# Performance work log

Hardware: AMD Instinct MI355X
Metric: run time of the kernel (lower is better)

Reference implementation:

```python
import jax, jax.numpy as jnp
import numpy as np

N_HEAD = 32
N_KV_HEAD = 8
HEAD_DIM = 64
N_EMBD = 2048
B, T = 2, 2048
ROPE_BASE = 10000.0


def _rope_cos_sin(T, head_dim, dtype):
    pos = jnp.arange(T, dtype=jnp.float32)
    dim_arr = jnp.arange(0, head_dim, 2, dtype=jnp.float32)
    freqs = ROPE_BASE ** (-dim_arr / head_dim)
    theta = jnp.outer(pos, freqs)                      # [T, hd/2]
    cos = jnp.concatenate([jnp.cos(theta), jnp.cos(theta)], axis=-1)  # [T, hd]
    sin = jnp.concatenate([jnp.sin(theta), jnp.sin(theta)], axis=-1)
    # broadcast to [1, T, 1, hd]
    return cos[None, :, None, :].astype(dtype), sin[None, :, None, :].astype(dtype)


def _rotate_half(v):
    h = v.shape[-1] // 2
    return jnp.concatenate([-v[..., h:], v[..., :h]], axis=-1)


def setup_inputs() -> dict:
    key = jax.random.key(0)
    kx, kq, kk, kv, ko = jax.random.split(key, 5)
    s = 1.0 / np.sqrt(N_EMBD)
    return {
        "x": jax.random.normal(kx, (B, T, N_EMBD), dtype=jnp.float32),
        "wq": jax.random.normal(kq, (N_EMBD, N_HEAD * HEAD_DIM), dtype=jnp.float32) * s,
        "wk": jax.random.normal(kk, (N_EMBD, N_KV_HEAD * HEAD_DIM), dtype=jnp.float32) * s,
        "wv": jax.random.normal(kv, (N_EMBD, N_KV_HEAD * HEAD_DIM), dtype=jnp.float32) * s,
        "wo": jax.random.normal(ko, (N_HEAD * HEAD_DIM, N_EMBD), dtype=jnp.float32) * s,
    }


def reference(x, wq, wk, wv, wo):
    Bx, Tx, C = x.shape
    n_rep = N_HEAD // N_KV_HEAD

    xq = (x @ wq).reshape(Bx, Tx, N_HEAD, HEAD_DIM)
    xk = (x @ wk).reshape(Bx, Tx, N_KV_HEAD, HEAD_DIM)
    xv = (x @ wv).reshape(Bx, Tx, N_KV_HEAD, HEAD_DIM)

    cos, sin = _rope_cos_sin(Tx, HEAD_DIM, x.dtype)
    xq = xq * cos + _rotate_half(xq) * sin
    xk = xk * cos + _rotate_half(xk) * sin

    # GQA: repeat_interleave KV heads to match query heads
    xk = jnp.repeat(xk, n_rep, axis=2)  # [B, T, H, hd]
    xv = jnp.repeat(xv, n_rep, axis=2)

    scale = 1.0 / np.sqrt(HEAD_DIM)
    # scores: [B, H, T, T]
    scores = jnp.einsum("bqhd,bkhd->bhqk", xq, xk) * scale
    causal = jnp.tril(jnp.ones((Tx, Tx), dtype=bool))
    scores = jnp.where(causal[None, None], scores, -jnp.inf)
    probs = jax.nn.softmax(scores, axis=-1)

    out = jnp.einsum("bhqk,bkhd->bqhd", probs, xv).reshape(Bx, Tx, N_HEAD * HEAD_DIM)
    return out @ wo
```

## Files before the change

### kernel.cpp

```cpp
#include <hip/hip_runtime.h>
#include <hip/hip_bf16.h>
#include <cstdint>
#include <cstddef>

#define B_ 2
#define T_ 2048
#define H_ 32
#define KVH_ 8
#define D_ 64
#define C_ 2048
#define NQKV 3072

typedef short short8 __attribute__((ext_vector_type(8)));
typedef float f32x4 __attribute__((ext_vector_type(4)));
typedef unsigned short u16;

__device__ __forceinline__ u16 f2b(float f) {
  union { float f; unsigned u; } x; x.f = f;
  unsigned r = x.u + 0x7fffu + ((x.u >> 16) & 1u);
  return (u16)(r >> 16);
}

__device__ __forceinline__ float b2f(u16 v) {
  union { unsigned u; float f; } x; x.u = ((unsigned)v) << 16;
  return x.f;
}

__device__ __forceinline__ void gload16(const void* g, void* l) {
  __builtin_amdgcn_global_load_lds(
      (const __attribute__((address_space(1))) unsigned int*)g,
      (__attribute__((address_space(3))) unsigned int*)l,
      16, 0, 0);
}

__device__ __forceinline__ f32x4 mfma16(short8 a, short8 b, f32x4 c) {
  return __builtin_amdgcn_mfma_f32_16x16x32_bf16(a, b, c, 0, 0, 0);
}

__device__ __forceinline__ unsigned cvtpk(float lo_, float hi_) {
  unsigned r;
  asm("v_cvt_pk_bf16_f32 %0, %1, %2" : "=v"(r) : "v"(lo_), "v"(hi_));
  return r;
}

__global__ void k_tbl(float* __restrict__ tbl) {
  int i = blockIdx.x * 256 + threadIdx.x;
  int t = i >> 5, f = i & 31;
  double freq = pow(10000.0, -(double)f / 32.0);
  double th = (double)t * freq;
  tbl[i * 2 + 0] = (float)cos(th);
  tbl[i * 2 + 1] = (float)sin(th);
}

__global__ void k_cvtx(const float* __restrict__ x, u16* __restrict__ xb) {
  int i = blockIdx.x * 256 + threadIdx.x;
  float4 v = ((const float4*)x)[i];
  ushort4 o;
  o.x = f2b(v.x); o.y = f2b(v.y); o.z = f2b(v.z); o.w = f2b(v.w);
  ((ushort4*)xb)[i] = o;
}

__global__ void k_transw(const float* __restrict__ src, u16* __restrict__ dst, int N) {
  __shared__ float t[32][33];
  int tx = threadIdx.x, ty = threadIdx.y;
  int k0 = blockIdx.y * 32, n0 = blockIdx.x * 32;
#pragma unroll
  for (int i = 0; i < 4; i++)
    t[ty + i * 8][tx] = src[(size_t)(k0 + ty + i * 8) * N + n0 + tx];
  __syncthreads();
#pragma unroll
  for (int i = 0; i < 4; i++) {
    int nl = ty + i * 8;
    dst[(size_t)(n0 + nl) * 2048 + k0 + tx] = f2b(t[tx][nl]);
  }
}

template <bool BF16OUT>
__global__ __launch_bounds__(256, 2) void k_gemm(const u16* __restrict__ A,
                                                 const u16* __restrict__ Bt,
                                                 void* __restrict__ Cc,
                                                 int M, int N, int K) {
  __shared__ __align__(16) u16 As[128 * 32];
  __shared__ __align__(16) u16 Bs[128 * 32];
  const int tid = threadIdx.x;
  const int w = tid >> 6, l = tid & 63;
  const int lo = l & 15, hi = l >> 4;
  const int m0 = blockIdx.y * 128, n0 = blockIdx.x * 128;
  const int wr = w >> 1, wc = w & 1;
  f32x4 acc[4][4];
#pragma unroll
  for (int i = 0; i < 4; i++)
#pragma unroll
    for (int j = 0; j < 4; j++) acc[i][j] = (f32x4){0.f, 0.f, 0.f, 0.f};

  for (int k0 = 0; k0 < K; k0 += 32) {
#pragma unroll
    for (int i = 0; i < 2; i++) {
      int cid = i * 256 + tid;
      int row = cid >> 2, kc = cid & 3;
      gload16(A + (size_t)(m0 + row) * K + k0 + kc * 8, &As[(i * 256 + w * 64) * 8]);
      gload16(Bt + (size_t)(n0 + row) * K + k0 + kc * 8, &Bs[(i * 256 + w * 64) * 8]);
    }
    __syncthreads();
    short8 a[4], b[4];
#pragma unroll
    for (int i = 0; i < 4; i++)
      a[i] = *(const short8*)&As[(wr * 64 + i * 16 + lo) * 32 + hi * 8];
#pragma unroll
    for (int j = 0; j < 4; j++)
      b[j] = *(const short8*)&Bs[(wc * 64 + j * 16 + lo) * 32 + hi * 8];
#pragma unroll
    for (int i = 0; i < 4; i++)
#pragma unroll
      for (int j = 0; j < 4; j++) acc[i][j] = mfma16(a[i], b[j], acc[i][j]);
    __syncthreads();
  }
  const int r0 = m0 + wr * 64, c0 = n0 + wc * 64;
#pragma unroll
  for (int i = 0; i < 4; i++)
#pragma unroll
    for (int j = 0; j < 4; j++) {
      f32x4 v = acc[i][j];
      int col = c0 + j * 16 + lo;
      int rw = r0 + i * 16 + hi * 4;
#pragma unroll
      for (int r = 0; r < 4; r++) {
        if (BF16OUT)
          ((u16*)Cc)[(size_t)(rw + r) * N + col] = f2b(v[r]);
        else
          ((float*)Cc)[(size_t)(rw + r) * N + col] = v[r];
      }
    }
}

__global__ void k_rope(const u16* __restrict__ QKV, const float* __restrict__ tbl,
                       u16* __restrict__ Qb, u16* __restrict__ Kb, u16* __restrict__ Vb) {
  int bt = blockIdx.x;
  int b = bt >> 11, t = bt & 2047;
  const u16* row = QKV + (size_t)bt * NQKV;
  const float2* cs = (const float2*)tbl + (size_t)t * 32;
  int tid = threadIdx.x;
  const float QS = 0.125f * 1.44269504089f;
#pragma unroll
  for (int i = 0; i < 4; i++) {
    int p = i * 256 + tid;
    int h = p >> 5, dd = p & 31;
    float2 c = cs[dd];
    float q0 = b2f(row[h * 64 + dd]), q1 = b2f(row[h * 64 + dd + 32]);
    float o0 = (q0 * c.x - q1 * c.y) * QS;
    float o1 = (q1 * c.x + q0 * c.y) * QS;
    size_t base = ((size_t)(b * H_ + h) * T_ + t) * 64 + dd;
    Qb[base] = f2b(o0);
    Qb[base + 32] = f2b(o1);
  }
  {
    int kvh = tid >> 5, dd = tid & 31;
    float2 c = cs[dd];
    float k0v = b2f(row[2048 + kvh * 64 + dd]), k1v = b2f(row[2048 + kvh * 64 + dd + 32]);
    size_t base = ((size_t)(b * KVH_ + kvh) * T_ + t) * 64 + dd;
    Kb[base] = f2b(k0v * c.x - k1v * c.y);
    Kb[base + 32] = f2b(k1v * c.x + k0v * c.y);
  }
#pragma unroll
  for (int i = 0; i < 2; i++) {
    int e = i * 256 + tid;
    int kvh = e >> 6, dd = e & 63;
    Vb[((size_t)(b * KVH_ + kvh) * T_ + t) * 64 + dd] = row[2560 + e];
  }
}

__global__ void k_vtrans(const u16* __restrict__ Vb, u16* __restrict__ Vt) {
  __shared__ u16 tl[64][65];
  int bk = blockIdx.y;
  int t0 = blockIdx.x * 64;
  int tid = threadIdx.x;
#pragma unroll
  for (int i = 0; i < 16; i++) {
    int e = i * 256 + tid;
    int tlc = e >> 6, d = e & 63;
    tl[tlc][d] = Vb[((size_t)bk * T_ + t0 + tlc) * 64 + d];
  }
  __syncthreads();
#pragma unroll
  for (int i = 0; i < 16; i++) {
    int e = i * 256 + tid;
    int d = e >> 6, tc = e & 63;
    Vt[((size_t)bk * 64 + d) * T_ + t0 + tc] = tl[tc][d];
  }
}

#define PSTR 40
__global__ __launch_bounds__(256)
__attribute__((amdgpu_waves_per_eu(3, 3)))
void k_attn(const u16* __restrict__ Qb,
            const u16* __restrict__ Kb,
            const u16* __restrict__ Vt,
            u16* __restrict__ Ob) {
  __shared__ __align__(16) u16 Pl[4][2][16 * PSTR];
  const int tid = threadIdx.x, w = tid >> 6, l = tid & 63;
  const int lo = l & 15, hi = l >> 4;
  const int b = blockIdx.z, h = blockIdx.y, kvh = h >> 2;
  const int p = (int)blockIdx.x * 4 + w;

  const size_t qbase = (size_t)(b * H_ + h) * T_ * 64;
  const size_t kbase = (size_t)(b * KVH_ + kvh) * T_ * 64;
  const size_t vbase = (size_t)(b * KVH_ + kvh) * 64 * T_;

  int q0;

  auto LOADK = [&](short8 (&ak)[2][2], int kv0) {
#pragma unroll
    for (int f = 0; f < 2; f++)
#pragma unroll
      for (int hf = 0; hf < 2; hf++)
        ak[f][hf] = *(const short8*)&Kb[kbase + (size_t)(kv0 + f * 16 + lo) * 64 + hf * 32 + hi * 8];
  };

  for (int pass = 0; pass < 2; pass++) {
    const int tile = pass ? (63 - p) : p;
    q0 = tile * 32;

    short8 aq[2][2];
#pragma unroll
    for (int qt = 0; qt < 2; qt++)
#pragma unroll
      for (int hf = 0; hf < 2; hf++)
        aq[qt][hf] = *(const short8*)&Qb[qbase + (size_t)(q0 + qt * 16 + lo) * 64 + hf * 32 + hi * 8];

    f32x4 o[2][4];
    float m[2], lsum[2];
#pragma unroll
    for (int qt = 0; qt < 2; qt++) {
      m[qt] = -1e30f; lsum[qt] = 0.f;
#pragma unroll
      for (int jd = 0; jd < 4; jd++) o[qt][jd] = (f32x4){0.f, 0.f, 0.f, 0.f};
    }

    auto STEP = [&](const short8 (&ak)[2][2], int kv0, bool masked) {
      short8 av[4];
#pragma unroll
      for (int jd = 0; jd < 4; jd++)
        av[jd] = *(const short8*)&Vt[vbase + (size_t)(jd * 16 + lo) * T_ + kv0 + hi * 8];

      f32x4 s[2][2];
      __builtin_amdgcn_s_setprio(1);
#pragma unroll
      for (int qt = 0; qt < 2; qt++)
#pragma unroll
        for (int f = 0; f < 2; f++) {
          f32x4 acc = (f32x4){0.f, 0.f, 0.f, 0.f};
          acc = mfma16(ak[f][0], aq[qt][0], acc);
          acc = mfma16(ak[f][1], aq[qt][1], acc);
          s[qt][f] = acc;
        }
      __builtin_amdgcn_s_setprio(0);

#pragma unroll
      for (int qt = 0; qt < 2; qt++) {
        const int myq = q0 + qt * 16 + lo;
        float p_[8];
#pragma unroll
        for (int f = 0; f < 2; f++)
#pragma unroll
          for (int r = 0; r < 4; r++) {
            float v = s[qt][f][r];
            if (masked) {
              int kv = kv0 + f * 16 + hi * 4 + r;
              v = (kv <= myq) ? v : -1e30f;
            }
            p_[f * 4 + r] = v;
          }
        float mx = fmaxf(fmaxf(fmaxf(p_[0], p_[1]), fmaxf(p_[2], p_[3])),
                         fmaxf(fmaxf(p_[4], p_[5]), fmaxf(p_[6], p_[7])));
        mx = fmaxf(mx, __shfl_xor(mx, 16));
        mx = fmaxf(mx, __shfl_xor(mx, 32));
        if (!__all(mx <= m[qt] + 11.5f)) {
          float mn = fmaxf(m[qt], mx);
          float a_ = exp2f(m[qt] - mn);
          m[qt] = mn;
          lsum[qt] *= a_;
#pragma unroll
          for (int jd = 0; jd < 4; jd++) {
            f32x4 t = o[qt][jd];
#pragma unroll
            for (int r = 0; r < 4; r++) t[r] *= a_;
            o[qt][jd] = t;
          }
        }
        float sm = 0.f;
#pragma unroll
        for (int i = 0; i < 8; i++) { p_[i] = exp2f(p_[i] - m[qt]); sm += p_[i]; }
        sm += __shfl_xor(sm, 16);
        sm += __shfl_xor(sm, 32);
        lsum[qt] += sm;
        uint2 w0, w1;
        w0.x = cvtpk(p_[0], p_[1]); w0.y = cvtpk(p_[2], p_[3]);
        w1.x = cvtpk(p_[4], p_[5]); w1.y = cvtpk(p_[6], p_[7]);
        *(uint2*)&Pl[w][qt][lo * PSTR + hi * 4] = w0;
        *(uint2*)&Pl[w][qt][lo * PSTR + 16 + hi * 4] = w1;
      }

#pragma unroll
      for (int qt = 0; qt < 2; qt++) {
        short8 pb = *(const short8*)&Pl[w][qt][lo * PSTR + hi * 8];
        __builtin_amdgcn_s_setprio(1);
#pragma unroll
        for (int jd = 0; jd < 4; jd++) o[qt][jd] = mfma16(av[jd], pb, o[qt][jd]);
        __builtin_amdgcn_s_setprio(0);
      }
    };

    short8 akA[2][2], akB[2][2];
    LOADK(akA, 0);
    int kv0 = 0;
    while (kv0 + 64 <= q0) {
      LOADK(akB, kv0 + 32);
      STEP(akA, kv0, false);
      LOADK(akA, kv0 + 64);
      STEP(akB, kv0 + 32, false);
      kv0 += 64;
    }
    if (kv0 < q0) {
      LOADK(akB, q0);
      STEP(akA, kv0, false);
      STEP(akB, q0, true);
    } else {
      STEP(akA, q0, true);
    }

#pragma unroll
    for (int qt = 0; qt < 2; qt++) {
      const int myq = q0 + qt * 16 + lo;
      float inv = 1.0f / lsum[qt];
      size_t obase = ((size_t)(b * T_ + myq) * H_ + h) * 64;
#pragma unroll
      for (int jd = 0; jd < 4; jd++) {
        ushort4 ov;
        ov.x = f2b(o[qt][jd][0] * inv);
        ov.y = f2b(o[qt][jd][1] * inv);
        ov.z = f2b(o[qt][jd][2] * inv);
        ov.w = f2b(o[qt][jd][3] * inv);
        *(ushort4*)&Ob[obase + jd * 16 + hi * 4] = ov;
      }
    }
  }
}

constexpr size_t OFF_TBL = 0;
constexpr size_t SZ_TBL = (size_t)T_ * 32 * 2 * 4;
constexpr size_t OFF_XB = OFF_TBL + SZ_TBL;
constexpr size_t SZ_XB = (size_t)B_ * T_ * C_ * 2;
constexpr size_t OFF_WQKVT = OFF_XB + SZ_XB;
constexpr size_t SZ_WQKVT = (size_t)NQKV * C_ * 2;
constexpr size_t OFF_WOT = OFF_WQKVT + SZ_WQKVT;
constexpr size_t SZ_WOT = (size_t)C_ * C_ * 2;
constexpr size_t OFF_QKV = OFF_WOT + SZ_WOT;
constexpr size_t SZ_QKV = (size_t)B_ * T_ * NQKV * 2;
constexpr size_t OFF_QB = OFF_QKV + SZ_QKV;
constexpr size_t SZ_QB = (size_t)B_ * H_ * T_ * D_ * 2;
constexpr size_t OFF_KB = OFF_QB + SZ_QB;
constexpr size_t SZ_KVB = (size_t)B_ * KVH_ * T_ * D_ * 2;
constexpr size_t OFF_VB = OFF_KB + SZ_KVB;
constexpr size_t OFF_VT = OFF_VB + SZ_KVB;
constexpr size_t OFF_OB = OFF_VT + SZ_KVB;
constexpr size_t SZ_OB = (size_t)B_ * T_ * H_ * D_ * 2;

extern "C" void kernel_launch(void* const* d_in, const int* in_sizes, int n_in,
                              void* d_out, int out_size, void* d_ws, size_t ws_size,
                              hipStream_t stream) {
  const float* x = (const float*)d_in[0];
  const float* wq = (const float*)d_in[1];
  const float* wk = (const float*)d_in[2];
  const float* wv = (const float*)d_in[3];
  const float* wo = (const float*)d_in[4];

  char* ws = (char*)d_ws;
  float* tbl = (float*)(ws + OFF_TBL);
  u16* xb = (u16*)(ws + OFF_XB);
  u16* wqkvT = (u16*)(ws + OFF_WQKVT);
  u16* woT = (u16*)(ws + OFF_WOT);
  u16* qkv = (u16*)(ws + OFF_QKV);
  u16* Qb = (u16*)(ws + OFF_QB);
  u16* Kb = (u16*)(ws + OFF_KB);
  u16* Vb = (u16*)(ws + OFF_VB);
  u16* Vt = (u16*)(ws + OFF_VT);
  u16* Ob = (u16*)(ws + OFF_OB);

  k_tbl<<<256, 256, 0, stream>>>(tbl);
  k_cvtx<<<8192, 256, 0, stream>>>(x, xb);
  dim3 tb(32, 8);
  k_transw<<<dim3(64, 64), tb, 0, stream>>>(wq, wqkvT, 2048);
  k_transw<<<dim3(16, 64), tb, 0, stream>>>(wk, wqkvT + (size_t)2048 * 2048, 512);
  k_transw<<<dim3(16, 64), tb, 0, stream>>>(wv, wqkvT + (size_t)2560 * 2048, 512);
  k_transw<<<dim3(64, 64), tb, 0, stream>>>(wo, woT, 2048);

  k_gemm<true><<<dim3(NQKV / 128, (B_ * T_) / 128), 256, 0, stream>>>(
      xb, wqkvT, qkv, B_ * T_, NQKV, C_);
  k_rope<<<B_ * T_, 256, 0, stream>>>(qkv, tbl, Qb, Kb, Vb);
  k_vtrans<<<dim3(T_ / 64, B_ * KVH_), 256, 0, stream>>>(Vb, Vt);
  k_attn<<<dim3(8, H_, B_), 256, 0, stream>>>(Qb, Kb, Vt, Ob);
  k_gemm<false><<<dim3(C_ / 128, (B_ * T_) / 128), 256, 0, stream>>>(
      Ob, woT, d_out, B_ * T_, C_, C_);
}
```

Measured before the change: 273.8 us.

## Fuse RoPE and V transpose into QKV GEMM epilogue; deepen K tile

The QKV projection GEMM epilogue now applies RoPE and the softmax scale directly to the accumulators. It writes Q and K in head-major layout and V already transposed. This removes the separate k_rope and k_vtrans kernels and the intermediate QKV and Vb buffers along with their global round-trips. The GEMM K-step also doubles from 32 to 64, halving the number of barriers per tile at the cost of more LDS. The epilogue writes are scattered 2-byte stores, which may coalesce poorly.

```diff
diff --git a/kernel.cpp b/kernel.cpp
--- a/kernel.cpp
+++ b/kernel.cpp
@@ -21,11 +21,6 @@
   return (u16)(r >> 16);
 }
 
-__device__ __forceinline__ float b2f(u16 v) {
-  union { unsigned u; float f; } x; x.u = ((unsigned)v) << 16;
-  return x.f;
-}
-
 __device__ __forceinline__ void gload16(const void* g, void* l) {
   __builtin_amdgcn_global_load_lds(
       (const __attribute__((address_space(1))) unsigned int*)g,
@@ -75,13 +70,17 @@
   }
 }
 
-template <bool BF16OUT>
+template <int MODE>
 __global__ __launch_bounds__(256, 2) void k_gemm(const u16* __restrict__ A,
                                                  const u16* __restrict__ Bt,
                                                  void* __restrict__ Cc,
-                                                 int M, int N, int K) {
-  __shared__ __align__(16) u16 As[128 * 32];
-  __shared__ __align__(16) u16 Bs[128 * 32];
+                                                 int M, int N, int K,
+                                                 const float* __restrict__ tbl,
+                                                 u16* __restrict__ Qb,
+                                                 u16* __restrict__ Kb,
+                                                 u16* __restrict__ Vt) {
+  __shared__ __align__(16) u16 As[128 * 64];
+  __shared__ __align__(16) u16 Bs[128 * 64];
   const int tid = threadIdx.x;
   const int w = tid >> 6, l = tid & 63;
   const int lo = l & 15, hi = l >> 4;
@@ -93,99 +92,83 @@
 #pragma unroll
     for (int j = 0; j < 4; j++) acc[i][j] = (f32x4){0.f, 0.f, 0.f, 0.f};
 
-  for (int k0 = 0; k0 < K; k0 += 32) {
-#pragma unroll
-    for (int i = 0; i < 2; i++) {
+  for (int k0 = 0; k0 < K; k0 += 64) {
+#pragma unroll
+    for (int i = 0; i < 4; i++) {
       int cid = i * 256 + tid;
-      int row = cid >> 2, kc = cid & 3;
+      int row = cid >> 3, kc = cid & 7;
       gload16(A + (size_t)(m0 + row) * K + k0 + kc * 8, &As[(i * 256 + w * 64) * 8]);
       gload16(Bt + (size_t)(n0 + row) * K + k0 + kc * 8, &Bs[(i * 256 + w * 64) * 8]);
     }
     __syncthreads();
-    short8 a[4], b[4];
-#pragma unroll
-    for (int i = 0; i < 4; i++)
-      a[i] = *(const short8*)&As[(wr * 64 + i * 16 + lo) * 32 + hi * 8];
-#pragma unroll
-    for (int j = 0; j < 4; j++)
-      b[j] = *(const short8*)&Bs[(wc * 64 + j * 16 + lo) * 32 + hi * 8];
-#pragma unroll
-    for (int i = 0; i < 4; i++)
-#pragma unroll
-      for (int j = 0; j < 4; j++) acc[i][j] = mfma16(a[i], b[j], acc[i][j]);
+#pragma unroll
+    for (int kk = 0; kk < 2; kk++) {
+      short8 a[4], b[4];
+#pragma unroll
+      for (int i = 0; i < 4; i++)
+        a[i] = *(const short8*)&As[(wr * 64 + i * 16 + lo) * 64 + kk * 32 + hi * 8];
+#pragma unroll
+      for (int j = 0; j < 4; j++)
+        b[j] = *(const short8*)&Bs[(wc * 64 + j * 16 + lo) * 64 + kk * 32 + hi * 8];
+#pragma unroll
+      for (int i = 0; i < 4; i++)
+#pragma unroll
+        for (int j = 0; j < 4; j++) acc[i][j] = mfma16(a[i], b[j], acc[i][j]);
+    }
     __syncthreads();
   }
   const int r0 = m0 + wr * 64, c0 = n0 + wc * 64;
-#pragma unroll
-  for (int i = 0; i < 4; i++)
-#pragma unroll
-    for (int j = 0; j < 4; j++) {
-      f32x4 v = acc[i][j];
-      int col = c0 + j * 16 + lo;
-      int rw = r0 + i * 16 + hi * 4;
-#pragma unroll
-      for (int r = 0; r < 4; r++) {
-        if (BF16OUT)
-          ((u16*)Cc)[(size_t)(rw + r) * N + col] = f2b(v[r]);
-        else
+
+  if (MODE == 0) {
+#pragma unroll
+    for (int i = 0; i < 4; i++)
+#pragma unroll
+      for (int j = 0; j < 4; j++) {
+        f32x4 v = acc[i][j];
+        int col = c0 + j * 16 + lo;
+        int rw = r0 + i * 16 + hi * 4;
+#pragma unroll
+        for (int r = 0; r < 4; r++)
           ((float*)Cc)[(size_t)(rw + r) * N + col] = v[r];
       }
-    }
-}
-
-__global__ void k_rope(const u16* __restrict__ QKV, const float* __restrict__ tbl,
-                       u16* __restrict__ Qb, u16* __restrict__ Kb, u16* __restrict__ Vb) {
-  int bt = blockIdx.x;
-  int b = bt >> 11, t = bt & 2047;
-  const u16* row = QKV + (size_t)bt * NQKV;
-  const float2* cs = (const float2*)tbl + (size_t)t * 32;
-  int tid = threadIdx.x;
-  const float QS = 0.125f * 1.44269504089f;
-#pragma unroll
-  for (int i = 0; i < 4; i++) {
-    int p = i * 256 + tid;
-    int h = p >> 5, dd = p & 31;
-    float2 c = cs[dd];
-    float q0 = b2f(row[h * 64 + dd]), q1 = b2f(row[h * 64 + dd + 32]);
-    float o0 = (q0 * c.x - q1 * c.y) * QS;
-    float o1 = (q1 * c.x + q0 * c.y) * QS;
-    size_t base = ((size_t)(b * H_ + h) * T_ + t) * 64 + dd;
-    Qb[base] = f2b(o0);
-    Qb[base + 32] = f2b(o1);
-  }
-  {
-    int kvh = tid >> 5, dd = tid & 31;
-    float2 c = cs[dd];
-    float k0v = b2f(row[2048 + kvh * 64 + dd]), k1v = b2f(row[2048 + kvh * 64 + dd + 32]);
-    size_t base = ((size_t)(b * KVH_ + kvh) * T_ + t) * 64 + dd;
-    Kb[base] = f2b(k0v * c.x - k1v * c.y);
-    Kb[base + 32] = f2b(k1v * c.x + k0v * c.y);
-  }
-#pragma unroll
-  for (int i = 0; i < 2; i++) {
-    int e = i * 256 + tid;
-    int kvh = e >> 6, dd = e & 63;
-    Vb[((size_t)(b * KVH_ + kvh) * T_ + t) * 64 + dd] = row[2560 + e];
-  }
-}
-
-__global__ void k_vtrans(const u16* __restrict__ Vb, u16* __restrict__ Vt) {
-  __shared__ u16 tl[64][65];
-  int bk = blockIdx.y;
-  int t0 = blockIdx.x * 64;
-  int tid = threadIdx.x;
-#pragma unroll
-  for (int i = 0; i < 16; i++) {
-    int e = i * 256 + tid;
-    int tlc = e >> 6, d = e & 63;
-    tl[tlc][d] = Vb[((size_t)bk * T_ + t0 + tlc) * 64 + d];
-  }
-  __syncthreads();
-#pragma unroll
-  for (int i = 0; i < 16; i++) {
-    int e = i * 256 + tid;
-    int d = e >> 6, tc = e & 63;
-    Vt[((size_t)bk * 64 + d) * T_ + t0 + tc] = tl[tc][d];
+  } else {
+    const int hd = c0 >> 6;
+    const int b = m0 >> 11;
+    if (hd < 40) {
+      const bool isQ = (hd < 32);
+      const float sc = isQ ? 0.125f * 1.44269504089f : 1.0f;
+      u16* dst = isQ ? (Qb + (size_t)(b * H_ + hd) * T_ * 64)
+                     : (Kb + (size_t)(b * KVH_ + (hd - 32)) * T_ * 64);
+#pragma unroll
+      for (int i = 0; i < 4; i++)
+#pragma unroll
+        for (int r = 0; r < 4; r++) {
+          int t = (r0 + i * 16 + hi * 4 + r) & (T_ - 1);
+          float2 cA = *(const float2*)&tbl[((size_t)t * 32 + lo) * 2];
+          float2 cB = *(const float2*)&tbl[((size_t)t * 32 + 16 + lo) * 2];
+          float a0 = acc[i][0][r], a1 = acc[i][1][r];
+          float a2 = acc[i][2][r], a3 = acc[i][3][r];
+          size_t rb = (size_t)t * 64;
+          dst[rb + lo]      = f2b((a0 * cA.x - a2 * cA.y) * sc);
+          dst[rb + 32 + lo] = f2b((a2 * cA.x + a0 * cA.y) * sc);
+          dst[rb + 16 + lo] = f2b((a1 * cB.x - a3 * cB.y) * sc);
+          dst[rb + 48 + lo] = f2b((a3 * cB.x + a1 * cB.y) * sc);
+        }
+    } else {
+      const int kvh = hd - 40;
+      u16* dst = Vt + (size_t)(b * KVH_ + kvh) * 64 * T_;
+#pragma unroll
+      for (int i = 0; i < 4; i++)
+#pragma unroll
+        for (int j = 0; j < 4; j++) {
+          int t = (r0 + i * 16 + hi * 4) & (T_ - 1);
+          int dd = j * 16 + lo;
+          f32x4 v = acc[i][j];
+          ushort4 ov;
+          ov.x = f2b(v[0]); ov.y = f2b(v[1]); ov.z = f2b(v[2]); ov.w = f2b(v[3]);
+          *(ushort4*)&dst[(size_t)dd * T_ + t] = ov;
+        }
+    }
   }
 }
 
@@ -206,8 +189,6 @@
   const size_t kbase = (size_t)(b * KVH_ + kvh) * T_ * 64;
   const size_t vbase = (size_t)(b * KVH_ + kvh) * 64 * T_;
 
-  int q0;
-
   auto LOADK = [&](short8 (&ak)[2][2], int kv0) {
 #pragma unroll
     for (int f = 0; f < 2; f++)
@@ -218,7 +199,7 @@
 
   for (int pass = 0; pass < 2; pass++) {
     const int tile = pass ? (63 - p) : p;
-    q0 = tile * 32;
+    const int q0 = tile * 32;
 
     short8 aq[2][2];
 #pragma unroll
@@ -354,14 +335,11 @@
 constexpr size_t SZ_WQKVT = (size_t)NQKV * C_ * 2;
 constexpr size_t OFF_WOT = OFF_WQKVT + SZ_WQKVT;
 constexpr size_t SZ_WOT = (size_t)C_ * C_ * 2;
-constexpr size_t OFF_QKV = OFF_WOT + SZ_WOT;
-constexpr size_t SZ_QKV = (size_t)B_ * T_ * NQKV * 2;
-constexpr size_t OFF_QB = OFF_QKV + SZ_QKV;
+constexpr size_t OFF_QB = OFF_WOT + SZ_WOT;
 constexpr size_t SZ_QB = (size_t)B_ * H_ * T_ * D_ * 2;
 constexpr size_t OFF_KB = OFF_QB + SZ_QB;
 constexpr size_t SZ_KVB = (size_t)B_ * KVH_ * T_ * D_ * 2;
-constexpr size_t OFF_VB = OFF_KB + SZ_KVB;
-constexpr size_t OFF_VT = OFF_VB + SZ_KVB;
+constexpr size_t OFF_VT = OFF_KB + SZ_KVB;
 constexpr size_t OFF_OB = OFF_VT + SZ_KVB;
 constexpr size_t SZ_OB = (size_t)B_ * T_ * H_ * D_ * 2;
 
@@ -379,10 +357,8 @@
   u16* xb = (u16*)(ws + OFF_XB);
   u16* wqkvT = (u16*)(ws + OFF_WQKVT);
   u16* woT = (u16*)(ws + OFF_WOT);
-  u16* qkv = (u16*)(ws + OFF_QKV);
   u16* Qb = (u16*)(ws + OFF_QB);
   u16* Kb = (u16*)(ws + OFF_KB);
-  u16* Vb = (u16*)(ws + OFF_VB);
   u16* Vt = (u16*)(ws + OFF_VT);
   u16* Ob = (u16*)(ws + OFF_OB);
 
@@ -394,11 +370,9 @@
   k_transw<<<dim3(16, 64), tb, 0, stream>>>(wv, wqkvT + (size_t)2560 * 2048, 512);
   k_transw<<<dim3(64, 64), tb, 0, stream>>>(wo, woT, 2048);
 
-  k_gemm<true><<<dim3(NQKV / 128, (B_ * T_) / 128), 256, 0, stream>>>(
-      xb, wqkvT, qkv, B_ * T_, NQKV, C_);
-  k_rope<<<B_ * T_, 256, 0, stream>>>(qkv, tbl, Qb, Kb, Vb);
-  k_vtrans<<<dim3(T_ / 64, B_ * KVH_), 256, 0, stream>>>(Vb, Vt);
+  k_gemm<1><<<dim3(NQKV / 128, (B_ * T_) / 128), 256, 0, stream>>>(
+      xb, wqkvT, nullptr, B_ * T_, NQKV, C_, tbl, Qb, Kb, Vt);
   k_attn<<<dim3(8, H_, B_), 256, 0, stream>>>(Qb, Kb, Vt, Ob);
-  k_gemm<false><<<dim3(C_ / 128, (B_ * T_) / 128), 256, 0, stream>>>(
-      Ob, woT, d_out, B_ * T_, C_, C_);
-}
+  k_gemm<0><<<dim3(C_ / 128, (B_ * T_) / 128), 256, 0, stream>>>(
+      Ob, woT, d_out, B_ * T_, C_, C_, nullptr, nullptr, nullptr, nullptr);
+}
```

Measured after the change: 263.9 us. 3.6% less time.
